# Kernel tuning notes

Measured on AMD Instinct MI355X. Metric: run time of the kernel, lower is better.

The kernel has to match this reference:

```python
import jax, jax.numpy as jnp
import numpy as np

D_MODEL = 2048
N_HEADS = 16
HEAD_DIM = D_MODEL // N_HEADS
D_FF = 4 * D_MODEL
B, L = 2, 2048
EPS = 1e-5


def _layernorm(x, g, b):
    mu = jnp.mean(x, axis=-1, keepdims=True)
    var = jnp.var(x, axis=-1, keepdims=True)
    return (x - mu) * jax.lax.rsqrt(var + EPS) * g + b


def setup_inputs() -> dict:
    key = jax.random.key(0)
    ks = jax.random.split(key, 8)
    s = 0.02
    x = jax.random.normal(ks[0], (B, L, D_MODEL), dtype=jnp.float32)
    # causal 4-D float mask [B,1,L,L]: 1 = attend, 0 = masked
    attention_mask = jnp.broadcast_to(
        jnp.tril(jnp.ones((L, L), dtype=jnp.float32))[None, None], (B, 1, L, L)
    )
    w_qkv = jax.random.normal(ks[1], (D_MODEL, 3 * D_MODEL), dtype=jnp.float32) * s
    w_o = jax.random.normal(ks[2], (D_MODEL, D_MODEL), dtype=jnp.float32) * s
    w1 = jax.random.normal(ks[3], (D_MODEL, D_FF), dtype=jnp.float32) * s
    b1 = jnp.zeros((D_FF,), dtype=jnp.float32)
    w2 = jax.random.normal(ks[4], (D_FF, D_MODEL), dtype=jnp.float32) * s
    b2 = jnp.zeros((D_MODEL,), dtype=jnp.float32)
    g_ln1 = jnp.ones((D_MODEL,), dtype=jnp.float32)
    b_ln1 = jnp.zeros((D_MODEL,), dtype=jnp.float32)
    g_ln2 = jnp.ones((D_MODEL,), dtype=jnp.float32)
    b_ln2 = jnp.zeros((D_MODEL,), dtype=jnp.float32)
    return {
        "x": x, "attention_mask": attention_mask,
        "w_qkv": w_qkv, "w_o": w_o,
        "g_ln1": g_ln1, "b_ln1": b_ln1, "g_ln2": g_ln2, "b_ln2": b_ln2,
        "w1": w1, "b1": b1, "w2": w2, "b2": b2,
    }


def reference(x, attention_mask, w_qkv, w_o, g_ln1, b_ln1, g_ln2, b_ln2, w1, b1, w2, b2):
    Bx, Lx, D = x.shape
    residual = x
    h = _layernorm(x, g_ln1, b_ln1)
    qkv = (h @ w_qkv).reshape(Bx, Lx, 3, N_HEADS, HEAD_DIM)
    q, k, v = jnp.moveaxis(qkv, 2, 0)           # each [B, L, H, Hd]
    q = q.transpose(0, 2, 1, 3)                  # [B, H, L, Hd]
    k = k.transpose(0, 2, 1, 3)
    v = v.transpose(0, 2, 1, 3)
    scores = jnp.einsum("bhqd,bhkd->bhqk", q, k) / np.float32(np.sqrt(HEAD_DIM))
    scores = scores + (1.0 - attention_mask) * -10000.0  # 4-D float mask branch
    attn = jax.nn.softmax(scores, axis=-1)
    out = jnp.einsum("bhqk,bhkd->bhqd", attn, v)
    out = out.transpose(0, 2, 1, 3).reshape(Bx, Lx, D)
    out = out @ w_o
    x2 = residual + out
    h2 = _layernorm(x2, g_ln2, b_ln2)
    mlp = jax.nn.gelu(h2 @ w1 + b1, approximate=False) @ w2 + b2
    return x2 + mlp
```

## Files before the change

### kernel.cpp

```cpp
#include <hip/hip_runtime.h>
#include <hip/hip_bf16.h>

#define DM   2048
#define LSEQ 2048
#define NB   2
#define NH   16
#define HDIM 128
#define DFF  8192

typedef __attribute__((ext_vector_type(8))) short bf16x8;
typedef __attribute__((ext_vector_type(4))) float f32x4;

typedef __attribute__((address_space(1))) void gvoid;
typedef __attribute__((address_space(3))) void lvoid;
#define GLDS16(g, s) __builtin_amdgcn_global_load_lds((const gvoid*)(g), (lvoid*)(s), 16, 0, 0)

__device__ __forceinline__ unsigned short f2b(float f) {
    __hip_bfloat16 h = __float2bfloat16(f);
    return *reinterpret_cast<unsigned short*>(&h);
}

__global__ __launch_bounds__(256) void transpose_bf16(const float* __restrict__ in,
                                                      unsigned short* __restrict__ out,
                                                      int R, int C) {
    __shared__ float t[32][33];
    const int c0 = blockIdx.x * 32, r0 = blockIdx.y * 32;
    const int tx = threadIdx.x, ty = threadIdx.y;
#pragma unroll
    for (int i = 0; i < 4; i++)
        t[ty + 8 * i][tx] = in[(size_t)(r0 + ty + 8 * i) * C + c0 + tx];
    __syncthreads();
#pragma unroll
    for (int i = 0; i < 4; i++)
        out[(size_t)(c0 + ty + 8 * i) * R + r0 + tx] = f2b(t[tx][ty + 8 * i]);
}

__global__ __launch_bounds__(256) void ln_k(const float* __restrict__ x,
                                            const float* __restrict__ g,
                                            const float* __restrict__ bta,
                                            unsigned short* __restrict__ out) {
    const int row = blockIdx.x, tid = threadIdx.x;
    const float* xr = x + (size_t)row * DM;
    float4 v0 = *(const float4*)&xr[tid * 4];
    float4 v1 = *(const float4*)&xr[1024 + tid * 4];
    float s  = v0.x + v0.y + v0.z + v0.w + v1.x + v1.y + v1.z + v1.w;
    float ss = v0.x * v0.x + v0.y * v0.y + v0.z * v0.z + v0.w * v0.w
             + v1.x * v1.x + v1.y * v1.y + v1.z * v1.z + v1.w * v1.w;
#pragma unroll
    for (int o = 32; o; o >>= 1) { s += __shfl_down(s, o); ss += __shfl_down(ss, o); }
    __shared__ float red[8];
    const int w = tid >> 6, l = tid & 63;
    if (l == 0) { red[w] = s; red[4 + w] = ss; }
    __syncthreads();
    s  = red[0] + red[1] + red[2] + red[3];
    ss = red[4] + red[5] + red[6] + red[7];
    const float mu  = s * (1.0f / DM);
    const float var = ss * (1.0f / DM) - mu * mu;
    const float rst = rsqrtf(var + 1e-5f);
    float4 g0 = *(const float4*)&g[tid * 4];
    float4 b0 = *(const float4*)&bta[tid * 4];
    float4 g1 = *(const float4*)&g[1024 + tid * 4];
    float4 b1 = *(const float4*)&bta[1024 + tid * 4];
    ushort4 o0, o1;
    o0.x = f2b((v0.x - mu) * rst * g0.x + b0.x);
    o0.y = f2b((v0.y - mu) * rst * g0.y + b0.y);
    o0.z = f2b((v0.z - mu) * rst * g0.z + b0.z);
    o0.w = f2b((v0.w - mu) * rst * g0.w + b0.w);
    o1.x = f2b((v1.x - mu) * rst * g1.x + b1.x);
    o1.y = f2b((v1.y - mu) * rst * g1.y + b1.y);
    o1.z = f2b((v1.z - mu) * rst * g1.z + b1.z);
    o1.w = f2b((v1.w - mu) * rst * g1.w + b1.w);
    *(ushort4*)&out[(size_t)row * DM + tid * 4] = o0;
    *(ushort4*)&out[(size_t)row * DM + 1024 + tid * 4] = o1;
}

template <bool BIAS, bool GELU_, bool RES, bool OUTBF>
__global__ __launch_bounds__(256) void gemm_k(const unsigned short* __restrict__ A,
                                              const unsigned short* __restrict__ Bt,
                                              const float* __restrict__ bias,
                                              const float* __restrict__ res,
                                              void* __restrict__ outp,
                                              int M, int N, int K) {
    __shared__ unsigned short Al[128 * 32];
    __shared__ unsigned short Bl[128 * 32];
    const int tid = threadIdx.x, w = tid >> 6, l = tid & 63;
    int bx = blockIdx.x, by = blockIdx.y;
    if (gridDim.x == 16 && gridDim.y == 32) {
        const int flat = by * 16 + bx;
        const int xx = flat & 7, jj = flat >> 3;
        by = 4 * xx + (jj & 3);
        bx = jj >> 2;
    }
    const int n0 = bx * 128, m0 = by * 128;
    const int wr = (w >> 1) * 64, wc = (w & 1) * 64;
    const int lr = l & 15, ko = (l >> 4) * 8;
    f32x4 acc[4][4] = {};

    const int srow = w * 32 + (l >> 2);
    const int skk  = (l & 3) * 8;
    const unsigned short* ga0 = A + (size_t)(m0 + srow) * K + skk;
    const unsigned short* ga1 = ga0 + (size_t)16 * K;
    const unsigned short* gb0 = Bt + (size_t)(n0 + srow) * K + skk;
    const unsigned short* gb1 = gb0 + (size_t)16 * K;
    unsigned short* la = &Al[w * 1024];
    unsigned short* lb = &Bl[w * 1024];
    const int nk = K >> 5;
    for (int kt = 0; kt < nk; ++kt) {
        GLDS16(ga0, la);
        GLDS16(ga1, la + 512);
        GLDS16(gb0, lb);
        GLDS16(gb1, lb + 512);
        ga0 += 32; ga1 += 32; gb0 += 32; gb1 += 32;
        __syncthreads();
        bf16x8 af[4], bv[4];
#pragma unroll
        for (int i = 0; i < 4; i++) af[i] = *(const bf16x8*)&Al[(wr + i * 16 + lr) * 32 + ko];
#pragma unroll
        for (int i = 0; i < 4; i++) bv[i] = *(const bf16x8*)&Bl[(wc + i * 16 + lr) * 32 + ko];
#pragma unroll
        for (int i = 0; i < 4; i++)
#pragma unroll
            for (int j = 0; j < 4; j++)
                acc[i][j] = __builtin_amdgcn_mfma_f32_16x16x32_bf16(af[i], bv[j], acc[i][j], 0, 0, 0);
        __syncthreads();
    }
#pragma unroll
    for (int j = 0; j < 4; j++) {
        const int col = n0 + wc + j * 16 + lr;
        const float bvv = BIAS ? bias[col] : 0.0f;
#pragma unroll
        for (int i = 0; i < 4; i++) {
#pragma unroll
            for (int r = 0; r < 4; r++) {
                const int row = m0 + wr + i * 16 + (l >> 4) * 4 + r;
                float v = acc[i][j][r] + bvv;
                if (GELU_) v = 0.5f * v * (1.0f + erff(v * 0.7071067811865476f));
                if (RES) v += res[(size_t)row * N + col];
                if (OUTBF) ((unsigned short*)outp)[(size_t)row * N + col] = f2b(v);
                else       ((float*)outp)[(size_t)row * N + col] = v;
            }
        }
    }
}

#define WAITVM4() asm volatile("s_waitcnt vmcnt(4)" ::: "memory")
#define WAITVM0() asm volatile("s_waitcnt vmcnt(0)" ::: "memory")
#define WAITLG()  asm volatile("s_waitcnt lgkmcnt(0)" ::: "memory")
#define BAR() __builtin_amdgcn_s_barrier()

template <int S, int HM>
__device__ __forceinline__ void read_a(const unsigned short* LDSu, bf16x8 (&af)[8],
                                       int wr, int lr, int k0x, int k1x) {
    const unsigned short* pa = LDSu + S * 16384 + wr * 8192;
#pragma unroll
    for (int mi = 0; mi < 4; mi++) {
        const int row = HM * 64 + mi * 16 + lr;
        af[mi * 2 + 0] = *(const bf16x8*)&pa[row * 64 + k0x];
        af[mi * 2 + 1] = *(const bf16x8*)&pa[row * 64 + k1x];
    }
}
template <int S, int HN>
__device__ __forceinline__ void read_b(const unsigned short* LDSu, bf16x8 (&bf)[4],
                                       int wc, int lr, int k0x, int k1x) {
    const unsigned short* pb = LDSu + 32768 + S * 16384 + (wc >> 1) * 8192;
#pragma unroll
    for (int nj = 0; nj < 2; nj++) {
        const int row = (wc & 1) * 64 + HN * 32 + nj * 16 + lr;
        bf[nj * 2 + 0] = *(const bf16x8*)&pb[row * 64 + k0x];
        bf[nj * 2 + 1] = *(const bf16x8*)&pb[row * 64 + k1x];
    }
}
template <int HM, int HN>
__device__ __forceinline__ void quad(f32x4 (&acc)[8][4], const bf16x8 (&af)[8],
                                     const bf16x8 (&bf)[4]) {
    __builtin_amdgcn_s_setprio(1);
#pragma unroll
    for (int mi = 0; mi < 4; mi++)
#pragma unroll
        for (int nj = 0; nj < 2; nj++)
#pragma unroll
            for (int ks = 0; ks < 2; ks++)
                acc[HM * 4 + mi][HN * 2 + nj] = __builtin_amdgcn_mfma_f32_16x16x32_bf16(
                    af[mi * 2 + ks], bf[nj * 2 + ks], acc[HM * 4 + mi][HN * 2 + nj], 0, 0, 0);
    __builtin_amdgcn_s_setprio(0);
}

template <bool BIAS, bool GELU_>
__global__ __launch_bounds__(512, 2) void gemm8_k(const unsigned short* __restrict__ A,
                                                  const unsigned short* __restrict__ Bt,
                                                  const float* __restrict__ bias,
                                                  unsigned short* __restrict__ out,
                                                  int N, int K, int nbx) {
    extern __shared__ unsigned short LDSu[];
    const int tid = threadIdx.x, w = tid >> 6, l = tid & 63;
    const int wr = w >> 2, wc = w & 3;
    const int lr = l & 15, lg = l >> 4;
    (void)nbx;
    const int id = blockIdx.x;
    const int x = id & 7, j = id >> 3;
    const int m0 = (2 * x + (j & 1)) * 256;
    const int n0 = (j >> 1) * 256;

    const int swx = (lr & 7) << 3;
    const int k0x = (lg * 8) ^ swx;
    const int k1x = k0x ^ 32;

    const int cs = tid ^ ((tid >> 3) & 7);
    const int sr = cs >> 3, sc = (cs & 7) * 8;
    const unsigned short* a0row = A + (size_t)(m0 + sr) * K + sc;
    const unsigned short* a1row = A + (size_t)(m0 + 128 + sr) * K + sc;
    const unsigned short* b0row = Bt + (size_t)(n0 + sr) * K + sc;
    const unsigned short* b1row = Bt + (size_t)(n0 + 128 + sr) * K + sc;
    const size_t row64 = (size_t)64 * K;

#define STAGE_A(S, H, ROW, KOFF) do { \
    GLDS16((ROW) + (KOFF),         LDSu + (S) * 16384 + (H) * 8192 + tid * 8); \
    GLDS16((ROW) + row64 + (KOFF), LDSu + (S) * 16384 + (H) * 8192 + 4096 + tid * 8); } while (0)
#define STAGE_B(S, H, ROW, KOFF) do { \
    GLDS16((ROW) + (KOFF),         LDSu + 32768 + (S) * 16384 + (H) * 8192 + tid * 8); \
    GLDS16((ROW) + row64 + (KOFF), LDSu + 32768 + (S) * 16384 + (H) * 8192 + 4096 + tid * 8); } while (0)

    f32x4 acc[8][4] = {};
    bf16x8 af[8], bf0[4], bf1[4];

    STAGE_A(0, 0, a0row, 0);
    STAGE_A(0, 1, a1row, 0);
    STAGE_B(0, 0, b0row, 0);
    STAGE_B(0, 1, b1row, 0);
    STAGE_B(1, 0, b0row, 64);
    STAGE_B(1, 1, b1row, 64);
    WAITVM4();
    BAR();

    const int niter = K >> 7;
    for (int i = 0; i < niter; ++i) {
        const bool last = (i == niter - 1);
        const int k1 = (2 * i + 1) * 64, k2 = k1 + 64, k3 = k1 + 128;
        read_a<0, 0>(LDSu, af, wr, lr, k0x, k1x);
        read_b<0, 0>(LDSu, bf0, wc, lr, k0x, k1x);
        STAGE_A(1, 0, a0row, k1);
        BAR(); quad<0, 0>(acc, af, bf0); BAR();
        read_b<0, 1>(LDSu, bf1, wc, lr, k0x, k1x);
        STAGE_A(1, 1, a1row, k1);
        BAR(); quad<0, 1>(acc, af, bf1); BAR();
        read_a<0, 1>(LDSu, af, wr, lr, k0x, k1x);
        if (!last) STAGE_B(0, 0, b0row, k2);
        BAR(); quad<1, 1>(acc, af, bf1); BAR();
        if (!last) { STAGE_B(0, 1, b1row, k2); WAITVM4(); } else { WAITVM0(); }
        BAR(); quad<1, 0>(acc, af, bf0); BAR();
        read_a<1, 0>(LDSu, af, wr, lr, k0x, k1x);
        read_b<1, 0>(LDSu, bf0, wc, lr, k0x, k1x);
        if (!last) STAGE_A(0, 0, a0row, k2);
        BAR(); quad<0, 0>(acc, af, bf0); BAR();
        read_b<1, 1>(LDSu, bf1, wc, lr, k0x, k1x);
        if (!last) STAGE_A(0, 1, a1row, k2);
        BAR(); quad<0, 1>(acc, af, bf1); BAR();
        read_a<1, 1>(LDSu, af, wr, lr, k0x, k1x);
        if (!last) STAGE_B(1, 0, b0row, k3);
        BAR(); quad<1, 1>(acc, af, bf1); BAR();
        if (!last) { STAGE_B(1, 1, b1row, k3); WAITVM4(); }
        BAR(); quad<1, 0>(acc, af, bf0); BAR();
    }

    float* eb = (float*)&LDSu[(size_t)w * 2176];
    const int row16 = l >> 2, ch = l & 3;
    float4 bv[4];
    if (BIAS) {
#pragma unroll
        for (int q = 0; q < 4; q++)
            bv[q] = *(const float4*)&bias[n0 + wc * 64 + ch * 16 + q * 4];
    }
#pragma unroll
    for (int mi8 = 0; mi8 < 8; ++mi8) {
        WAITLG();
        __builtin_amdgcn_sched_barrier(0);
#pragma unroll
        for (int nj = 0; nj < 4; nj++)
#pragma unroll
            for (int rr = 0; rr < 4; rr++)
                eb[(lg * 4 + rr) * 68 + nj * 16 + lr] = acc[mi8][nj][rr];
        WAITLG();
        __builtin_amdgcn_sched_barrier(0);
        alignas(16) unsigned short tmp[16];
#pragma unroll
        for (int q = 0; q < 4; q++) {
            float4 v = *(const float4*)&eb[row16 * 68 + ch * 16 + q * 4];
            float e0 = v.x, e1 = v.y, e2 = v.z, e3 = v.w;
            if (BIAS) { e0 += bv[q].x; e1 += bv[q].y; e2 += bv[q].z; e3 += bv[q].w; }
            if (GELU_) {
                e0 = 0.5f * e0 * (1.0f + erff(e0 * 0.7071067811865476f));
                e1 = 0.5f * e1 * (1.0f + erff(e1 * 0.7071067811865476f));
                e2 = 0.5f * e2 * (1.0f + erff(e2 * 0.7071067811865476f));
                e3 = 0.5f * e3 * (1.0f + erff(e3 * 0.7071067811865476f));
            }
            tmp[q * 4 + 0] = f2b(e0); tmp[q * 4 + 1] = f2b(e1);
            tmp[q * 4 + 2] = f2b(e2); tmp[q * 4 + 3] = f2b(e3);
        }
        unsigned short* dst = out + (size_t)(m0 + wr * 128 + mi8 * 16 + row16) * N
                              + n0 + wc * 64 + ch * 16;
        *(uint4*)dst = *(const uint4*)tmp;
        *(uint4*)(dst + 8) = *(const uint4*)(tmp + 8);
    }
#undef STAGE_A
#undef STAGE_B
}

__global__ __launch_bounds__(256) void flash_attn_k(const unsigned short* __restrict__ qkv,
                                                    unsigned short* __restrict__ out) {
    __shared__ unsigned short Kl[64 * 136];
    __shared__ unsigned short Vt[128 * 64];
    __shared__ unsigned short Pl[4][16 * 72];
    const int tid = threadIdx.x, w = tid >> 6, l = tid & 63;
    const int bh = blockIdx.y, b = bh >> 4, h = bh & 15;
    const int lr = l & 15, lg = l >> 4;
    const float sc = 0.08838834764831845f;
    const int NT = LSEQ / 64;

#pragma unroll 1
    for (int pi = 0; pi < 2; ++pi) {
        const int qt = (pi == 0) ? (int)blockIdx.x : (NT - 1 - (int)blockIdx.x);
        const int qw = qt * 64 + w * 16;

        bf16x8 qf[4];
        {
            const unsigned short* qb = qkv + (size_t)(b * LSEQ + qw + lr) * (3 * DM) + h * HDIM + lg * 8;
#pragma unroll
            for (int kc = 0; kc < 4; kc++) qf[kc] = *(const bf16x8*)(qb + kc * 32);
        }
        f32x4 O[8] = {};
        float m_run[4] = {-1e30f, -1e30f, -1e30f, -1e30f};
        float l_run[4] = {};

        for (int kt = 0; kt <= qt; ++kt) {
            const int k0 = kt * 64;
#pragma unroll
            for (int i = 0; i < 4; i++) {
                const int seg = i * 256 + tid;
                const int row = seg >> 4;
                const int c8  = (seg & 15) * 8;
                const unsigned short* src = qkv + (size_t)(b * LSEQ + k0 + row) * (3 * DM) + DM + h * HDIM + c8;
                *(uint4*)&Kl[row * 136 + c8] = *(const uint4*)src;
                unsigned short tmp[8];
                *(uint4*)tmp = *(const uint4*)(src + DM);
#pragma unroll
                for (int j = 0; j < 8; j++) {
                    const int d = c8 + j;
                    Vt[d * 64 + (row ^ ((((d >> 3) ^ d) & 7) << 3))] = tmp[j];
                }
            }
            __syncthreads();
            f32x4 S[4] = {};
#pragma unroll
            for (int st = 0; st < 4; ++st)
#pragma unroll
                for (int kc = 0; kc < 4; kc++) {
                    bf16x8 kb = *(const bf16x8*)&Kl[(st * 16 + lr) * 136 + kc * 32 + lg * 8];
                    S[st] = __builtin_amdgcn_mfma_f32_16x16x32_bf16(qf[kc], kb, S[st], 0, 0, 0);
                }
            const bool lastt = (kt == qt);
#pragma unroll
            for (int rq = 0; rq < 4; rq++) {
                const int row = qw + lg * 4 + rq;
                float s0 = S[0][rq] * sc, s1 = S[1][rq] * sc, s2 = S[2][rq] * sc, s3 = S[3][rq] * sc;
                if (lastt) {
                    if (k0 +  0 + lr > row) s0 = -1e30f;
                    if (k0 + 16 + lr > row) s1 = -1e30f;
                    if (k0 + 32 + lr > row) s2 = -1e30f;
                    if (k0 + 48 + lr > row) s3 = -1e30f;
                }
                float mt = fmaxf(fmaxf(s0, s1), fmaxf(s2, s3));
                mt = fmaxf(mt, __shfl_xor(mt, 1));
                mt = fmaxf(mt, __shfl_xor(mt, 2));
                mt = fmaxf(mt, __shfl_xor(mt, 4));
                mt = fmaxf(mt, __shfl_xor(mt, 8));
                const float mn = fmaxf(m_run[rq], mt);
                const float al = __expf(m_run[rq] - mn);
                m_run[rq] = mn;
                float p0 = __expf(s0 - mn), p1 = __expf(s1 - mn), p2 = __expf(s2 - mn), p3 = __expf(s3 - mn);
                float ts = p0 + p1 + p2 + p3;
                ts += __shfl_xor(ts, 1);
                ts += __shfl_xor(ts, 2);
                ts += __shfl_xor(ts, 4);
                ts += __shfl_xor(ts, 8);
                l_run[rq] = l_run[rq] * al + ts;
#pragma unroll
                for (int c = 0; c < 8; c++) O[c][rq] *= al;
                unsigned short* pr = &Pl[w][(lg * 4 + rq) * 72 + lr];
                pr[0] = f2b(p0); pr[16] = f2b(p1); pr[32] = f2b(p2); pr[48] = f2b(p3);
            }
#pragma unroll
            for (int ks = 0; ks < 2; ++ks) {
                bf16x8 pa = *(const bf16x8*)&Pl[w][lr * 72 + ks * 32 + lg * 8];
#pragma unroll
                for (int c = 0; c < 8; c++) {
                    const int d = c * 16 + lr;
                    bf16x8 vb = *(const bf16x8*)&Vt[d * 64 + ((ks * 32 + lg * 8) ^ ((((d >> 3) ^ d) & 7) << 3))];
                    O[c] = __builtin_amdgcn_mfma_f32_16x16x32_bf16(pa, vb, O[c], 0, 0, 0);
                }
            }
            __syncthreads();
        }
#pragma unroll
        for (int rq = 0; rq < 4; rq++) {
            const float inv = 1.0f / l_run[rq];
            const size_t ro = (size_t)(b * LSEQ + qw + lg * 4 + rq) * DM + h * HDIM;
#pragma unroll
            for (int c = 0; c < 8; c++) out[ro + c * 16 + lr] = f2b(O[c][rq] * inv);
        }
    }
}

extern "C" void kernel_launch(void* const* d_in, const int* in_sizes, int n_in,
                              void* d_out, int out_size, void* d_ws, size_t ws_size,
                              hipStream_t stream) {
    const float* x     = (const float*)d_in[0];
    const float* w_qkv = (const float*)d_in[2];
    const float* w_o   = (const float*)d_in[3];
    const float* g1    = (const float*)d_in[4];
    const float* bl1   = (const float*)d_in[5];
    const float* g2    = (const float*)d_in[6];
    const float* bl2   = (const float*)d_in[7];
    const float* w1    = (const float*)d_in[8];
    const float* b1    = (const float*)d_in[9];
    const float* w2    = (const float*)d_in[10];
    const float* b2    = (const float*)d_in[11];
    float* out = (float*)d_out;

    unsigned char* p = (unsigned char*)d_ws;
    unsigned short* wqkvT = (unsigned short*)p; p += (size_t)3 * DM * DM * 2;
    unsigned short* woT   = (unsigned short*)p; p += (size_t)DM * DM * 2;
    unsigned short* w1T   = (unsigned short*)p; p += (size_t)DFF * DM * 2;
    unsigned short* w2T   = (unsigned short*)p; p += (size_t)DM * DFF * 2;
    unsigned short* hbuf  = (unsigned short*)p; p += (size_t)NB * LSEQ * DM * 2;
    unsigned short* big   = (unsigned short*)p; p += (size_t)NB * LSEQ * DFF * 2;
    float* x2 = out;

    const int R = NB * LSEQ;
    dim3 tb(32, 8);
    transpose_bf16<<<dim3(3 * DM / 32, DM / 32), tb, 0, stream>>>(w_qkv, wqkvT, DM, 3 * DM);
    transpose_bf16<<<dim3(DM / 32, DM / 32), tb, 0, stream>>>(w_o, woT, DM, DM);
    transpose_bf16<<<dim3(DFF / 32, DM / 32), tb, 0, stream>>>(w1, w1T, DM, DFF);
    transpose_bf16<<<dim3(DM / 32, DFF / 32), tb, 0, stream>>>(w2, w2T, DFF, DM);

    ln_k<<<R, 256, 0, stream>>>(x, g1, bl1, hbuf);
    gemm8_k<false, false><<<(R / 256) * (3 * DM / 256), 512, 131072, stream>>>(
        hbuf, wqkvT, nullptr, big, 3 * DM, DM, 3 * DM / 256);
    flash_attn_k<<<dim3(LSEQ / 128, NB * NH), 256, 0, stream>>>(big, hbuf);
    gemm_k<false, false, true, false><<<dim3(DM / 128, R / 128), 256, 0, stream>>>(
        hbuf, woT, nullptr, x, x2, R, DM, DM);
    ln_k<<<R, 256, 0, stream>>>(x2, g2, bl2, hbuf);
    gemm8_k<true, true><<<(R / 256) * (DFF / 256), 512, 131072, stream>>>(
        hbuf, w1T, b1, big, DFF, DM, DFF / 256);
    gemm_k<true, false, true, false><<<dim3(DM / 128, R / 128), 256, 0, stream>>>(
        big, w2T, b2, x2, out, R, DM, DFF);
}
```

Baseline: 811.6 us.

## Merge GEMM main-loop quad phases to halve block barriers per iteration

The bf16 MFMA GEMM main loop pairs consecutive quad compute phases into four larger phases instead of eight. LDS fragment reads and global-to-LDS staging for both halves are now issued together ahead of each merged phase. s_setprio now wraps each merged pair of quads rather than each single quad. The aim is to cut workgroup barrier count and synchronization stalls, at the cost of less fine-grained interleaving of loads with MFMA work and possibly longer exposed load latency per phase.

Measured after the change: 806.2 us. No clear change (-0.7%).

```diff
diff --git a/kernel.cpp b/kernel.cpp
--- a/kernel.cpp
+++ b/kernel.cpp
@@ -173,7 +173,6 @@
 template <int HM, int HN>
 __device__ __forceinline__ void quad(f32x4 (&acc)[8][4], const bf16x8 (&af)[8],
                                      const bf16x8 (&bf)[4]) {
-    __builtin_amdgcn_s_setprio(1);
 #pragma unroll
     for (int mi = 0; mi < 4; mi++)
 #pragma unroll
@@ -182,7 +181,6 @@
             for (int ks = 0; ks < 2; ks++)
                 acc[HM * 4 + mi][HN * 2 + nj] = __builtin_amdgcn_mfma_f32_16x16x32_bf16(
                     af[mi * 2 + ks], bf[nj * 2 + ks], acc[HM * 4 + mi][HN * 2 + nj], 0, 0, 0);
-    __builtin_amdgcn_s_setprio(0);
 }
 
 template <bool BIAS, bool GELU_>
@@ -238,28 +236,54 @@
         const int k1 = (2 * i + 1) * 64, k2 = k1 + 64, k3 = k1 + 128;
         read_a<0, 0>(LDSu, af, wr, lr, k0x, k1x);
         read_b<0, 0>(LDSu, bf0, wc, lr, k0x, k1x);
+        read_b<0, 1>(LDSu, bf1, wc, lr, k0x, k1x);
         STAGE_A(1, 0, a0row, k1);
-        BAR(); quad<0, 0>(acc, af, bf0); BAR();
-        read_b<0, 1>(LDSu, bf1, wc, lr, k0x, k1x);
         STAGE_A(1, 1, a1row, k1);
-        BAR(); quad<0, 1>(acc, af, bf1); BAR();
+        BAR();
+        __builtin_amdgcn_s_setprio(1);
+        quad<0, 0>(acc, af, bf0);
+        quad<0, 1>(acc, af, bf1);
+        __builtin_amdgcn_s_setprio(0);
+        BAR();
         read_a<0, 1>(LDSu, af, wr, lr, k0x, k1x);
-        if (!last) STAGE_B(0, 0, b0row, k2);
-        BAR(); quad<1, 1>(acc, af, bf1); BAR();
-        if (!last) { STAGE_B(0, 1, b1row, k2); WAITVM4(); } else { WAITVM0(); }
-        BAR(); quad<1, 0>(acc, af, bf0); BAR();
+        if (!last) {
+            STAGE_B(0, 0, b0row, k2);
+            STAGE_B(0, 1, b1row, k2);
+            WAITVM4();
+        } else {
+            WAITVM0();
+        }
+        BAR();
+        __builtin_amdgcn_s_setprio(1);
+        quad<1, 1>(acc, af, bf1);
+        quad<1, 0>(acc, af, bf0);
+        __builtin_amdgcn_s_setprio(0);
+        BAR();
         read_a<1, 0>(LDSu, af, wr, lr, k0x, k1x);
         read_b<1, 0>(LDSu, bf0, wc, lr, k0x, k1x);
-        if (!last) STAGE_A(0, 0, a0row, k2);
-        BAR(); quad<0, 0>(acc, af, bf0); BAR();
         read_b<1, 1>(LDSu, bf1, wc, lr, k0x, k1x);
-        if (!last) STAGE_A(0, 1, a1row, k2);
-        BAR(); quad<0, 1>(acc, af, bf1); BAR();
+        if (!last) {
+            STAGE_A(0, 0, a0row, k2);
+            STAGE_A(0, 1, a1row, k2);
+        }
+        BAR();
+        __builtin_amdgcn_s_setprio(1);
+        quad<0, 0>(acc, af, bf0);
+        quad<0, 1>(acc, af, bf1);
+        __builtin_amdgcn_s_setprio(0);
+        BAR();
         read_a<1, 1>(LDSu, af, wr, lr, k0x, k1x);
-        if (!last) STAGE_B(1, 0, b0row, k3);
-        BAR(); quad<1, 1>(acc, af, bf1); BAR();
-        if (!last) { STAGE_B(1, 1, b1row, k3); WAITVM4(); }
-        BAR(); quad<1, 0>(acc, af, bf0); BAR();
+        if (!last) {
+            STAGE_B(1, 0, b0row, k3);
+            STAGE_B(1, 1, b1row, k3);
+            WAITVM4();
+        }
+        BAR();
+        __builtin_amdgcn_s_setprio(1);
+        quad<1, 1>(acc, af, bf1);
+        quad<1, 0>(acc, af, bf0);
+        __builtin_amdgcn_s_setprio(0);
+        BAR();
     }
 
     float* eb = (float*)&LDSu[(size_t)w * 2176];
```
